# Performance work log

Hardware: AMD Instinct MI355X
Metric: run time of the kernel (lower is better)

## Reference

```python
import jax, jax.numpy as jnp
import numpy as np

EMBED = 256; M = 8; DV = 32; L = 4; K = 4; SCALE = 0.5
LEVELS = [(128, 128), (64, 64), (32, 32), (16, 16)]  # (H_l, W_l), static
S_TOTAL = sum(h * w for h, w in LEVELS)  # 21760


def _linear_params(key, fan_in, fan_out):
    kw, kb = jax.random.split(key)
    lim = 1.0 / np.sqrt(fan_in)
    W = jax.random.uniform(kw, (fan_in, fan_out), minval=-lim, maxval=lim, dtype=jnp.float32)
    b = jax.random.uniform(kb, (fan_out,), minval=-lim, maxval=lim, dtype=jnp.float32)
    return W, b


def setup_inputs() -> dict:
    key = jax.random.key(0)
    ks = jax.random.split(key, 8)
    N, Q = 2, 8192
    W_off, b_off = _linear_params(ks[0], EMBED, M * L * K * 2)
    W_attn, b_attn = _linear_params(ks[1], EMBED, M * L * K)
    W_val, b_val = _linear_params(ks[2], EMBED, M * DV)
    W_out, b_out = _linear_params(ks[3], M * DV, EMBED)
    queries = jax.random.normal(ks[4], (N, Q, EMBED), dtype=jnp.float32)
    query_geometry_logits = jax.random.normal(ks[5], (N, Q, 4), dtype=jnp.float32)
    value = jax.random.normal(ks[6], (N, S_TOTAL, EMBED), dtype=jnp.float32)
    value_mask = jnp.ones((N, S_TOTAL, 1), dtype=jnp.float32)
    return {"queries": queries, "query_geometry_logits": query_geometry_logits,
            "value": value, "value_mask": value_mask,
            "W_off": W_off, "b_off": b_off, "W_attn": W_attn, "b_attn": b_attn,
            "W_val": W_val, "b_val": b_val, "W_out": W_out, "b_out": b_out}


def _bilinear(img_flat, grid, H, W):
    """grid_sample(mode=bilinear, padding=zeros, align_corners=False).
    img_flat: (B, H*W, C); grid: (B, P, 2) with (x, y) in [-1, 1]."""
    x = (grid[..., 0] + 1.0) * (W * 0.5) - 0.5
    y = (grid[..., 1] + 1.0) * (H * 0.5) - 0.5
    x0f, y0f = jnp.floor(x), jnp.floor(y)
    wx, wy = x - x0f, y - y0f
    x0, y0 = x0f.astype(jnp.int32), y0f.astype(jnp.int32)

    def gather(xi, yi, w):
        valid = (xi >= 0) & (xi < W) & (yi >= 0) & (yi < H)
        idx = jnp.clip(yi, 0, H - 1) * W + jnp.clip(xi, 0, W - 1)
        v = jnp.take_along_axis(img_flat, idx[..., None], axis=1)
        return v * (w * valid)[..., None]

    return (gather(x0, y0, (1 - wx) * (1 - wy)) + gather(x0 + 1, y0, wx * (1 - wy))
            + gather(x0, y0 + 1, (1 - wx) * wy) + gather(x0 + 1, y0 + 1, wx * wy))


def _forward(queries, query_geometry_logits, value, value_mask,
             W_off, b_off, W_attn, b_attn, W_val, b_val, W_out, b_out):
    N, Q, _ = queries.shape
    # attention weights: (N, Q, M, L*K), softmax over the L*K sampling points
    attn = jax.nn.softmax((queries @ W_attn + b_attn).reshape(N, Q, M, L * K), axis=-1)
    # sampling offsets: (N, Q, M, L*K, 2)
    deltas = (queries @ W_off + b_off).reshape(N, Q, M, L * K, 2)
    # reference boxes: sigmoid -> (cx, cy, w, h) in [0, 1]
    b_q = jax.nn.sigmoid(query_geometry_logits)
    xy, wh = b_q[..., :2], b_q[..., 2:]
    scale = wh * (1.0 / K) * SCALE                       # (N, Q, 2)
    pos = xy[:, :, None, None, :] + deltas * scale[:, :, None, None, :]  # (N,Q,M,LK,2)
    # value projection + mask
    v_masked = value_mask * (value @ W_val + b_val)      # (N, S, M*DV)
    # collapse (N, M) for per-head grid sampling
    grid = jnp.clip(2.0 * pos.transpose(0, 2, 1, 3, 4).reshape(N * M, Q, L * K, 2) - 1.0, -1.0, 1.0)
    outs, start = [], 0
    for li, (H, W) in enumerate(LEVELS):
        v_l = v_masked[:, start:start + H * W, :].reshape(N, H * W, M, DV)
        v_l = v_l.transpose(0, 2, 1, 3).reshape(N * M, H * W, DV)
        g_l = grid[:, :, K * li:K * (li + 1), :].reshape(N * M, Q * K, 2)
        s_l = _bilinear(v_l, g_l, H, W)                  # (N*M, Q*K, DV)
        outs.append(s_l.reshape(N, M, Q, K, DV))
        start += H * W
    vals = jnp.concatenate(outs, axis=3)                 # (N, M, Q, L*K, DV)
    vals = vals.transpose(0, 2, 1, 3, 4)                 # (N, Q, M, L*K, DV)
    out = jnp.sum(attn[..., None] * vals, axis=3).reshape(N, Q, M * DV)
    return out @ W_out + b_out                           # (N, Q, EMBED)


def reference(queries, query_geometry_logits, value, value_mask,
              W_off, b_off, W_attn, b_attn, W_val, b_val, W_out, b_out):
    return _forward(queries, query_geometry_logits, value, value_mask,
                    W_off, b_off, W_attn, b_attn, W_val, b_val, W_out, b_out)
```

## Files before the change

### kernel.cpp

```cpp
#include <hip/hip_runtime.h>
#include <math.h>

#define EMBED   256
#define M_HEADS 8
#define DVAL    32
#define LK      16
#define S_TOTAL 21760
#define NQ      8192
#define NROWS   (2 * NQ)
#define QBS     16

typedef __attribute__((ext_vector_type(8))) short s16x8;
typedef __attribute__((ext_vector_type(4))) short s16x4;
typedef __attribute__((ext_vector_type(4))) float f32x4;
typedef unsigned short u16;
typedef unsigned int   u32;

__device__ __forceinline__ short f2bf(float f) {
    unsigned u = __float_as_uint(f);
    u += 0x7fffu + ((u >> 16) & 1u);
    return (short)(u >> 16);
}
__device__ __forceinline__ float bf2f(short h) {
    return __uint_as_float(((unsigned)(u16)h) << 16);
}

#define V_OFF     0
#define V_FLTS    5570560
#define PA_OFF    (V_OFF + V_FLTS)
#define PA_FLTS   6291456
#define MID_OFF   (PA_OFF + PA_FLTS)
#define MID_FLTS  2097152
#define WHI_OFF   (MID_OFF + MID_FLTS)
#define WOA_FLTS  49152
#define WLO_OFF   (WHI_OFF + WOA_FLTS)
#define WV_OFF    (WLO_OFF + WOA_FLTS)
#define WO_OFF    (WV_OFF + 32768)

__global__ __launch_bounds__(256) void prep_kernel(
    const float* __restrict__ W_off, const float* __restrict__ W_attn,
    u16* __restrict__ Whi,           u16* __restrict__ Wlo,
    const float* __restrict__ W_val, u16* __restrict__ Wv,
    const float* __restrict__ W_out, u16* __restrict__ Wo)
{
    const int b = blockIdx.x;
    const int t = threadIdx.x;

    if (b < 512) {
        const int flat = b * 256 + t;
        const int which = flat >> 16;
        const int e = flat & 65535;
        const int k = e >> 8, c = e & 255;
        const float f = which ? W_out[k * 256 + c] : W_val[k * 256 + c];
        const int kt = k >> 5, qd = (k >> 3) & 3, j = k & 7;
        const int idx = (((kt * 256 + c) << 2) + qd) * 8 + j;
        (which ? Wo : Wv)[idx] = (u16)f2bf(f);
    } else {
        const int flat = (b - 512) * 256 + t;
        const int k = flat / 384, c = flat - k * 384;
        const float f = (c < 256) ? W_off[k * 256 + c] : W_attn[k * 128 + (c - 256)];
        const short h = f2bf(f);
        const short lo = f2bf(f - bf2f(h));
        const int kt = k >> 5, qd = (k >> 3) & 3, j = k & 7;
        const int idx = (((kt * 384 + c) << 2) + qd) * 8 + j;
        Whi[idx] = (u16)h;
        Wlo[idx] = (u16)lo;
    }
}

__global__ __launch_bounds__(256, 2) void vproj_kernel(
    const float* __restrict__ value,
    const float* __restrict__ vmask,
    const u16* __restrict__ Wpk,
    const float* __restrict__ b_val,
    u16* __restrict__ v_out)
{
    __shared__ u16 sA[4096];

    const int t  = threadIdx.x;
    const int w  = t >> 6, l = t & 63;
    const int c  = l & 15, qd = l >> 4;
    const int c0 = w * 64;

    s16x8 B[8][4];
    #pragma unroll
    for (int kt = 0; kt < 8; ++kt)
        #pragma unroll
        for (int nt = 0; nt < 4; ++nt)
            B[kt][nt] = *(const s16x8*)(Wpk + (((kt * 256 + c0 + nt * 16 + c) << 2) + qd) * 8);

    float bias[4];
    #pragma unroll
    for (int nt = 0; nt < 4; ++nt) bias[nt] = b_val[c0 + nt * 16 + c];

    const int srow = t >> 6;
    const int scol = 4 * (t & 63);

    int tile = blockIdx.x;
    float4 st[4];
    {
        const float* __restrict__ vp = value + (size_t)tile * 16 * EMBED;
        #pragma unroll
        for (int i = 0; i < 4; ++i)
            st[i] = *(const float4*)(vp + (i * 4 + srow) * EMBED + scol);
    }

    for (;;) {
        #pragma unroll
        for (int i = 0; i < 4; ++i) {
            const int row = i * 4 + srow;
            const int idx = ((row << 8) + scol) ^ ((row & 7) << 3);
            *(s16x4*)(sA + idx) = (s16x4){ f2bf(st[i].x), f2bf(st[i].y),
                                           f2bf(st[i].z), f2bf(st[i].w) };
        }
        __syncthreads();

        const int r0   = tile * 16;
        const int next = tile + 512;
        if (next < 2720) {
            const float* __restrict__ vp = value + (size_t)next * 16 * EMBED;
            #pragma unroll
            for (int i = 0; i < 4; ++i)
                st[i] = *(const float4*)(vp + (i * 4 + srow) * EMBED + scol);
        }

        f32x4 acc[4] = {};
        #pragma unroll
        for (int kt = 0; kt < 8; ++kt) {
            const s16x8 a = *(const s16x8*)(sA + ((((c << 8) + kt * 32 + qd * 8)) ^ ((c & 7) << 3)));
            #pragma unroll
            for (int nt = 0; nt < 4; ++nt)
                acc[nt] = __builtin_amdgcn_mfma_f32_16x16x32_bf16(a, B[kt][nt], acc[nt], 0, 0, 0);
        }

        #pragma unroll
        for (int r = 0; r < 4; ++r) {
            const int grow = r0 + qd * 4 + r;
            const int n = (grow >= S_TOTAL) ? 1 : 0;
            const int s = grow - n * S_TOTAL;
            const float mk = vmask[grow];
            #pragma unroll
            for (int nt = 0; nt < 4; ++nt) {
                const int col = c0 + nt * 16 + c;
                const int hm = col >> 5, d = col & 31;
                v_out[((size_t)(n * M_HEADS + hm) * S_TOTAL + s) * DVAL + d] =
                    (u16)f2bf((acc[nt][r] + bias[nt]) * mk);
            }
        }
        __syncthreads();
        if (next >= 2720) break;
        tile = next;
    }
}

__global__ __launch_bounds__(256) void qproj_kernel(
    const float* __restrict__ queries,
    const float* __restrict__ qgl,
    const u16* __restrict__ Whi, const u16* __restrict__ Wlo,
    const float* __restrict__ b_off, const float* __restrict__ b_attn,
    float* __restrict__ pa)
{
    __shared__ __align__(16) char s_un[33280];
    __shared__ float s_attn[32][132];
    __shared__ float s_geom[32][4];

    u16* sAh = (u16*)s_un;
    u16* sAl = sAh + 8192;
    float (*s_off)[260] = (float(*)[260])s_un;

    const int t  = threadIdx.x;
    const int w  = t >> 6, l = t & 63;
    const int c  = l & 15, qd = l >> 4;
    const int row0 = blockIdx.x * 32;
    const int c0 = w * 96;

    if (t < 32) {
        const float* g = &qgl[(size_t)(row0 + t) * 4];
        s_geom[t][0] = 1.f / (1.f + __expf(-g[0]));
        s_geom[t][1] = 1.f / (1.f + __expf(-g[1]));
        s_geom[t][2] = (1.f / (1.f + __expf(-g[2]))) * 0.125f;
        s_geom[t][3] = (1.f / (1.f + __expf(-g[3]))) * 0.125f;
    }

    {
        const int srow = t >> 6;
        const int scol = 4 * (t & 63);
        #pragma unroll
        for (int i = 0; i < 8; ++i) {
            const int row = i * 4 + srow;
            const float4 v = *(const float4*)(queries + (size_t)(row0 + row) * EMBED + scol);
            const short h0 = f2bf(v.x), h1 = f2bf(v.y), h2 = f2bf(v.z), h3 = f2bf(v.w);
            const int idx = ((row << 8) + scol) ^ ((row & 7) << 3);
            *(s16x4*)(sAh + idx) = (s16x4){ h0, h1, h2, h3 };
            *(s16x4*)(sAl + idx) = (s16x4){ f2bf(v.x - bf2f(h0)), f2bf(v.y - bf2f(h1)),
                                            f2bf(v.z - bf2f(h2)), f2bf(v.w - bf2f(h3)) };
        }
    }
    __syncthreads();

    f32x4 acc[2][6] = {};

    s16x8 bhA[6], blA[6], bhB[6], blB[6];

    auto loadB = [&](int kt, s16x8 (&bh)[6], s16x8 (&bl)[6]) {
        #pragma unroll
        for (int nt = 0; nt < 6; ++nt) {
            const int idx = (((kt * 384 + c0 + nt * 16 + c) << 2) + qd) * 8;
            bh[nt] = *(const s16x8*)(Whi + idx);
            bl[nt] = *(const s16x8*)(Wlo + idx);
        }
    };
    auto stepK = [&](int kt, s16x8 (&bh)[6], s16x8 (&bl)[6]) {
        s16x8 ah[2], al[2];
        #pragma unroll
        for (int mt = 0; mt < 2; ++mt) {
            const int row = mt * 16 + c;
            const int idx = ((row << 8) + kt * 32 + qd * 8) ^ ((row & 7) << 3);
            ah[mt] = *(const s16x8*)(sAh + idx);
            al[mt] = *(const s16x8*)(sAl + idx);
        }
        #pragma unroll
        for (int mt = 0; mt < 2; ++mt)
            #pragma unroll
            for (int nt = 0; nt < 6; ++nt) {
                acc[mt][nt] = __builtin_amdgcn_mfma_f32_16x16x32_bf16(ah[mt], bh[nt], acc[mt][nt], 0, 0, 0);
                acc[mt][nt] = __builtin_amdgcn_mfma_f32_16x16x32_bf16(ah[mt], bl[nt], acc[mt][nt], 0, 0, 0);
                acc[mt][nt] = __builtin_amdgcn_mfma_f32_16x16x32_bf16(al[mt], bh[nt], acc[mt][nt], 0, 0, 0);
            }
    };

    loadB(0, bhA, blA);
    loadB(1, bhB, blB);
    #pragma unroll
    for (int kp = 0; kp < 4; ++kp) {
        stepK(2 * kp, bhA, blA);
        if (kp < 3) loadB(2 * kp + 2, bhA, blA);
        stepK(2 * kp + 1, bhB, blB);
        if (kp < 3) loadB(2 * kp + 3, bhB, blB);
    }
    __syncthreads();

    #pragma unroll
    for (int mt = 0; mt < 2; ++mt)
        #pragma unroll
        for (int nt = 0; nt < 6; ++nt) {
            const int col = c0 + nt * 16 + c;
            #pragma unroll
            for (int r = 0; r < 4; ++r) {
                const int row = mt * 16 + qd * 4 + r;
                if (col < 256) s_off[row][col] = acc[mt][nt][r] + b_off[col];
                else           s_attn[row][col - 256] = acc[mt][nt][r] + b_attn[col - 256];
            }
        }
    __syncthreads();

    {
        const int qi = t >> 3, hm = t & 7;
        float* a = &s_attn[qi][hm * LK];
        float mx = a[0];
        #pragma unroll
        for (int i = 1; i < LK; ++i) mx = fmaxf(mx, a[i]);
        float s = 0.f;
        #pragma unroll
        for (int i = 0; i < LK; ++i) { const float e = __expf(a[i] - mx); a[i] = e; s += e; }
        const float inv = 1.f / s;
        #pragma unroll
        for (int i = 0; i < LK; ++i) a[i] *= inv;
    }
    __syncthreads();

    for (int p = t; p < 32 * 128; p += 256) {
        const int qi = p >> 7;
        const int pt = p & 127;
        const int lvl = (pt & 15) >> 2;
        const float Wl = (float)(128 >> lvl);
        const float px = fmaf(s_off[qi][2 * pt + 0], s_geom[qi][2], s_geom[qi][0]);
        const float py = fmaf(s_off[qi][2 * pt + 1], s_geom[qi][3], s_geom[qi][1]);
        const float gx = fminf(fmaxf(2.f * px - 1.f, -1.f), 1.f);
        const float gy = fminf(fmaxf(2.f * py - 1.f, -1.f), 1.f);
        const float x = (gx + 1.f) * (Wl * 0.5f) - 0.5f;
        const float y = (gy + 1.f) * (Wl * 0.5f) - 0.5f;
        const size_t idx = ((size_t)(row0 + qi) * 128 + pt) * 3;
        pa[idx + 0] = x;
        pa[idx + 1] = y;
        pa[idx + 2] = s_attn[qi][pt];
    }
}

__global__ __launch_bounds__(256) void sample_kernel(
    const float* __restrict__ pa,
    const u16* __restrict__ v_tab,
    u16* __restrict__ mid)
{
    __shared__ int4   s_idx[QBS * 17];
    __shared__ float4 s_w[QBS * 17];

    const int t    = threadIdx.x;
    const int m    = blockIdx.x & 7;
    const int rest = blockIdx.x >> 3;
    const int qc   = rest & 511;
    const int n    = rest >> 9;
    const int q0   = qc * QBS;

    {
        const int qi = t >> 4, lk = t & 15;
        const int lvl   = lk >> 2;
        const int Wl    = 128 >> lvl;
        const int start = (lvl == 0) ? 0 : (lvl == 1) ? 16384 : (lvl == 2) ? 20480 : 21504;

        const size_t prow = ((size_t)(n * NQ + q0 + qi)) * 128 + m * 16 + lk;
        const float x  = pa[prow * 3 + 0];
        const float y  = pa[prow * 3 + 1];
        const float aw = pa[prow * 3 + 2];

        const float x0f = floorf(x), y0f = floorf(y);
        const int   x0 = (int)x0f, y0 = (int)y0f;
        const float wx = x - x0f, wy = y - y0f;

        const float vx0 = (x0 >= 0) ? 1.f : 0.f;
        const float vx1 = (x0 + 1 <= Wl - 1) ? 1.f : 0.f;
        const float vy0 = (y0 >= 0) ? 1.f : 0.f;
        const float vy1 = (y0 + 1 <= Wl - 1) ? 1.f : 0.f;

        const int xc0 = max(x0, 0);
        const int xc1 = min(x0 + 1, Wl - 1);
        const int yc0 = max(y0, 0);
        const int yc1 = min(y0 + 1, Wl - 1);

        const int e = qi * 17 + lk;
        s_idx[e] = make_int4((start + yc0 * Wl + xc0) * DVAL,
                             (start + yc0 * Wl + xc1) * DVAL,
                             (start + yc1 * Wl + xc0) * DVAL,
                             (start + yc1 * Wl + xc1) * DVAL);
        s_w[e] = make_float4(aw * (1.f - wx) * (1.f - wy) * vx0 * vy0,
                             aw * wx * (1.f - wy) * vx1 * vy0,
                             aw * (1.f - wx) * wy * vx0 * vy1,
                             aw * wx * wy * vx1 * vy1);
    }
    __syncthreads();

    const int g = t >> 4, dp = t & 15;
    const u16* __restrict__ vbp =
        v_tab + (size_t)(n * M_HEADS + m) * S_TOTAL * DVAL + 2 * dp;

    float acc0 = 0.f, acc1 = 0.f;
    #pragma unroll
    for (int lk = 0; lk < LK; ++lk) {
        const int4   id = s_idx[g * 17 + lk];
        const float4 w  = s_w[g * 17 + lk];
        const u32 u0 = *(const u32*)(vbp + id.x);
        const u32 u1 = *(const u32*)(vbp + id.y);
        const u32 u2 = *(const u32*)(vbp + id.z);
        const u32 u3 = *(const u32*)(vbp + id.w);
        acc0 = fmaf(w.x, __uint_as_float(u0 << 16), acc0);
        acc1 = fmaf(w.x, __uint_as_float(u0 & 0xffff0000u), acc1);
        acc0 = fmaf(w.y, __uint_as_float(u1 << 16), acc0);
        acc1 = fmaf(w.y, __uint_as_float(u1 & 0xffff0000u), acc1);
        acc0 = fmaf(w.z, __uint_as_float(u2 << 16), acc0);
        acc1 = fmaf(w.z, __uint_as_float(u2 & 0xffff0000u), acc1);
        acc0 = fmaf(w.w, __uint_as_float(u3 << 16), acc0);
        acc1 = fmaf(w.w, __uint_as_float(u3 & 0xffff0000u), acc1);
    }

    const u32 packed = ((u32)(u16)f2bf(acc1) << 16) | (u32)(u16)f2bf(acc0);
    *(u32*)(mid + ((size_t)(n * NQ + q0 + g)) * EMBED + m * DVAL + 2 * dp) = packed;
}

__global__ __launch_bounds__(256, 2) void out_kernel(
    const u16* __restrict__ mid,
    const u16* __restrict__ Wpk,
    const float* __restrict__ b_out,
    float* __restrict__ out)
{
    const int t  = threadIdx.x;
    const int w  = t >> 6, l = t & 63;
    const int c  = l & 15, qd = l >> 4;
    const int c0 = w * 64;

    s16x8 B[8][4];
    #pragma unroll
    for (int kt = 0; kt < 8; ++kt)
        #pragma unroll
        for (int nt = 0; nt < 4; ++nt)
            B[kt][nt] = *(const s16x8*)(Wpk + (((kt * 256 + c0 + nt * 16 + c) << 2) + qd) * 8);

    float bias[4];
    #pragma unroll
    for (int nt = 0; nt < 4; ++nt) bias[nt] = b_out[c0 + nt * 16 + c];

    for (int tile = blockIdx.x; tile < 1024; tile += 512) {
        const int r0 = tile * 16;
        const u16* __restrict__ ap = mid + (size_t)(r0 + c) * EMBED + qd * 8;

        s16x8 a[8];
        #pragma unroll
        for (int kt = 0; kt < 8; ++kt)
            a[kt] = *(const s16x8*)(ap + kt * 32);

        f32x4 acc[4] = {};
        #pragma unroll
        for (int kt = 0; kt < 8; ++kt)
            #pragma unroll
            for (int nt = 0; nt < 4; ++nt)
                acc[nt] = __builtin_amdgcn_mfma_f32_16x16x32_bf16(a[kt], B[kt][nt], acc[nt], 0, 0, 0);

        #pragma unroll
        for (int r = 0; r < 4; ++r) {
            const int row = r0 + qd * 4 + r;
            #pragma unroll
            for (int nt = 0; nt < 4; ++nt)
                out[(size_t)row * EMBED + c0 + nt * 16 + c] = acc[nt][r] + bias[nt];
        }
    }
}

extern "C" void kernel_launch(void* const* d_in, const int* in_sizes, int n_in,
                              void* d_out, int out_size, void* d_ws, size_t ws_size,
                              hipStream_t stream) {
    (void)in_sizes; (void)n_in; (void)out_size; (void)ws_size;

    const float* queries = (const float*)d_in[0];
    const float* qgl     = (const float*)d_in[1];
    const float* value   = (const float*)d_in[2];
    const float* vmask   = (const float*)d_in[3];
    const float* W_off   = (const float*)d_in[4];
    const float* b_off   = (const float*)d_in[5];
    const float* W_attn  = (const float*)d_in[6];
    const float* b_attn  = (const float*)d_in[7];
    const float* W_val   = (const float*)d_in[8];
    const float* b_val   = (const float*)d_in[9];
    const float* W_out   = (const float*)d_in[10];
    const float* b_out   = (const float*)d_in[11];

    float* ws   = (float*)d_ws;
    u16*  v_ws  = (u16*)(ws + V_OFF);
    float* pa   = ws + PA_OFF;
    u16*  mid   = (u16*)(ws + MID_OFF);
    u16*  whi   = (u16*)(ws + WHI_OFF);
    u16*  wlo   = (u16*)(ws + WLO_OFF);
    u16*  wvpk  = (u16*)(ws + WV_OFF);
    u16*  wopk  = (u16*)(ws + WO_OFF);
    float* outp = (float*)d_out;

    prep_kernel<<<896, 256, 0, stream>>>(W_off, W_attn, whi, wlo,
                                         W_val, wvpk, W_out, wopk);

    vproj_kernel<<<512, 256, 0, stream>>>(value, vmask, wvpk, b_val, v_ws);
    qproj_kernel<<<NROWS / 32, 256, 0, stream>>>(queries, qgl, whi, wlo,
                                                 b_off, b_attn, pa);
    sample_kernel<<<2 * (NQ / QBS) * M_HEADS, 256, 0, stream>>>(pa, v_ws, mid);
    out_kernel<<<512, 256, 0, stream>>>(mid, wopk, b_out, outp);
}
```

Before: 186.7 us.

## Merge value and query projection kernels into one launch with interleaved blocks

Fuses the value projection and query projection kernels into a single kernel, with even blocks doing value tiles and odd blocks doing query tiles. The aim is to overlap the two independent phases on the GPU and remove one launch and its tail. In exchange the value branch now shares a larger static LDS allocation and loses its launch_bounds occupancy hint, which may cut occupancy for those blocks.

```diff
diff --git a/kernel.cpp b/kernel.cpp
--- a/kernel.cpp
+++ b/kernel.cpp
@@ -68,222 +68,220 @@
     }
 }
 
-__global__ __launch_bounds__(256, 2) void vproj_kernel(
+__global__ __launch_bounds__(256) void vq_kernel(
     const float* __restrict__ value,
     const float* __restrict__ vmask,
-    const u16* __restrict__ Wpk,
+    const u16* __restrict__ Wvpk,
     const float* __restrict__ b_val,
-    u16* __restrict__ v_out)
-{
-    __shared__ u16 sA[4096];
-
-    const int t  = threadIdx.x;
-    const int w  = t >> 6, l = t & 63;
-    const int c  = l & 15, qd = l >> 4;
-    const int c0 = w * 64;
-
-    s16x8 B[8][4];
-    #pragma unroll
-    for (int kt = 0; kt < 8; ++kt)
-        #pragma unroll
-        for (int nt = 0; nt < 4; ++nt)
-            B[kt][nt] = *(const s16x8*)(Wpk + (((kt * 256 + c0 + nt * 16 + c) << 2) + qd) * 8);
-
-    float bias[4];
-    #pragma unroll
-    for (int nt = 0; nt < 4; ++nt) bias[nt] = b_val[c0 + nt * 16 + c];
-
-    const int srow = t >> 6;
-    const int scol = 4 * (t & 63);
-
-    int tile = blockIdx.x;
-    float4 st[4];
-    {
-        const float* __restrict__ vp = value + (size_t)tile * 16 * EMBED;
-        #pragma unroll
-        for (int i = 0; i < 4; ++i)
-            st[i] = *(const float4*)(vp + (i * 4 + srow) * EMBED + scol);
-    }
-
-    for (;;) {
-        #pragma unroll
-        for (int i = 0; i < 4; ++i) {
-            const int row = i * 4 + srow;
-            const int idx = ((row << 8) + scol) ^ ((row & 7) << 3);
-            *(s16x4*)(sA + idx) = (s16x4){ f2bf(st[i].x), f2bf(st[i].y),
-                                           f2bf(st[i].z), f2bf(st[i].w) };
-        }
-        __syncthreads();
-
-        const int r0   = tile * 16;
-        const int next = tile + 512;
-        if (next < 2720) {
-            const float* __restrict__ vp = value + (size_t)next * 16 * EMBED;
-            #pragma unroll
-            for (int i = 0; i < 4; ++i)
-                st[i] = *(const float4*)(vp + (i * 4 + srow) * EMBED + scol);
-        }
-
-        f32x4 acc[4] = {};
-        #pragma unroll
-        for (int kt = 0; kt < 8; ++kt) {
-            const s16x8 a = *(const s16x8*)(sA + ((((c << 8) + kt * 32 + qd * 8)) ^ ((c & 7) << 3)));
-            #pragma unroll
-            for (int nt = 0; nt < 4; ++nt)
-                acc[nt] = __builtin_amdgcn_mfma_f32_16x16x32_bf16(a, B[kt][nt], acc[nt], 0, 0, 0);
-        }
-
-        #pragma unroll
-        for (int r = 0; r < 4; ++r) {
-            const int grow = r0 + qd * 4 + r;
-            const int n = (grow >= S_TOTAL) ? 1 : 0;
-            const int s = grow - n * S_TOTAL;
-            const float mk = vmask[grow];
-            #pragma unroll
-            for (int nt = 0; nt < 4; ++nt) {
-                const int col = c0 + nt * 16 + c;
-                const int hm = col >> 5, d = col & 31;
-                v_out[((size_t)(n * M_HEADS + hm) * S_TOTAL + s) * DVAL + d] =
-                    (u16)f2bf((acc[nt][r] + bias[nt]) * mk);
-            }
-        }
-        __syncthreads();
-        if (next >= 2720) break;
-        tile = next;
-    }
-}
-
-__global__ __launch_bounds__(256) void qproj_kernel(
+    u16* __restrict__ v_out,
     const float* __restrict__ queries,
     const float* __restrict__ qgl,
     const u16* __restrict__ Whi, const u16* __restrict__ Wlo,
     const float* __restrict__ b_off, const float* __restrict__ b_attn,
     float* __restrict__ pa)
 {
-    __shared__ __align__(16) char s_un[33280];
-    __shared__ float s_attn[32][132];
-    __shared__ float s_geom[32][4];
-
-    u16* sAh = (u16*)s_un;
-    u16* sAl = sAh + 8192;
-    float (*s_off)[260] = (float(*)[260])s_un;
+    __shared__ __align__(16) char lds[50688];
 
     const int t  = threadIdx.x;
     const int w  = t >> 6, l = t & 63;
     const int c  = l & 15, qd = l >> 4;
-    const int row0 = blockIdx.x * 32;
-    const int c0 = w * 96;
-
-    if (t < 32) {
-        const float* g = &qgl[(size_t)(row0 + t) * 4];
-        s_geom[t][0] = 1.f / (1.f + __expf(-g[0]));
-        s_geom[t][1] = 1.f / (1.f + __expf(-g[1]));
-        s_geom[t][2] = (1.f / (1.f + __expf(-g[2]))) * 0.125f;
-        s_geom[t][3] = (1.f / (1.f + __expf(-g[3]))) * 0.125f;
-    }
-
-    {
+
+    if ((blockIdx.x & 1) == 0) {
+        u16* sA = (u16*)lds;
+
+        const int vb = blockIdx.x >> 1;
+        const int c0 = w * 64;
+
+        s16x8 B[8][4];
+        #pragma unroll
+        for (int kt = 0; kt < 8; ++kt)
+            #pragma unroll
+            for (int nt = 0; nt < 4; ++nt)
+                B[kt][nt] = *(const s16x8*)(Wvpk + (((kt * 256 + c0 + nt * 16 + c) << 2) + qd) * 8);
+
+        float bias[4];
+        #pragma unroll
+        for (int nt = 0; nt < 4; ++nt) bias[nt] = b_val[c0 + nt * 16 + c];
+
         const int srow = t >> 6;
         const int scol = 4 * (t & 63);
-        #pragma unroll
-        for (int i = 0; i < 8; ++i) {
-            const int row = i * 4 + srow;
-            const float4 v = *(const float4*)(queries + (size_t)(row0 + row) * EMBED + scol);
-            const short h0 = f2bf(v.x), h1 = f2bf(v.y), h2 = f2bf(v.z), h3 = f2bf(v.w);
-            const int idx = ((row << 8) + scol) ^ ((row & 7) << 3);
-            *(s16x4*)(sAh + idx) = (s16x4){ h0, h1, h2, h3 };
-            *(s16x4*)(sAl + idx) = (s16x4){ f2bf(v.x - bf2f(h0)), f2bf(v.y - bf2f(h1)),
-                                            f2bf(v.z - bf2f(h2)), f2bf(v.w - bf2f(h3)) };
-        }
-    }
-    __syncthreads();
-
-    f32x4 acc[2][6] = {};
-
-    s16x8 bhA[6], blA[6], bhB[6], blB[6];
-
-    auto loadB = [&](int kt, s16x8 (&bh)[6], s16x8 (&bl)[6]) {
-        #pragma unroll
-        for (int nt = 0; nt < 6; ++nt) {
-            const int idx = (((kt * 384 + c0 + nt * 16 + c) << 2) + qd) * 8;
-            bh[nt] = *(const s16x8*)(Whi + idx);
-            bl[nt] = *(const s16x8*)(Wlo + idx);
-        }
-    };
-    auto stepK = [&](int kt, s16x8 (&bh)[6], s16x8 (&bl)[6]) {
-        s16x8 ah[2], al[2];
-        #pragma unroll
-        for (int mt = 0; mt < 2; ++mt) {
-            const int row = mt * 16 + c;
-            const int idx = ((row << 8) + kt * 32 + qd * 8) ^ ((row & 7) << 3);
-            ah[mt] = *(const s16x8*)(sAh + idx);
-            al[mt] = *(const s16x8*)(sAl + idx);
-        }
+
+        int tile = vb;
+        float4 st[4];
+        {
+            const float* __restrict__ vp = value + (size_t)tile * 16 * EMBED;
+            #pragma unroll
+            for (int i = 0; i < 4; ++i)
+                st[i] = *(const float4*)(vp + (i * 4 + srow) * EMBED + scol);
+        }
+
+        for (;;) {
+            #pragma unroll
+            for (int i = 0; i < 4; ++i) {
+                const int row = i * 4 + srow;
+                const int idx = ((row << 8) + scol) ^ ((row & 7) << 3);
+                *(s16x4*)(sA + idx) = (s16x4){ f2bf(st[i].x), f2bf(st[i].y),
+                                               f2bf(st[i].z), f2bf(st[i].w) };
+            }
+            __syncthreads();
+
+            const int r0   = tile * 16;
+            const int next = tile + 512;
+            if (next < 2720) {
+                const float* __restrict__ vp = value + (size_t)next * 16 * EMBED;
+                #pragma unroll
+                for (int i = 0; i < 4; ++i)
+                    st[i] = *(const float4*)(vp + (i * 4 + srow) * EMBED + scol);
+            }
+
+            f32x4 acc[4] = {};
+            #pragma unroll
+            for (int kt = 0; kt < 8; ++kt) {
+                const s16x8 a = *(const s16x8*)(sA + ((((c << 8) + kt * 32 + qd * 8)) ^ ((c & 7) << 3)));
+                #pragma unroll
+                for (int nt = 0; nt < 4; ++nt)
+                    acc[nt] = __builtin_amdgcn_mfma_f32_16x16x32_bf16(a, B[kt][nt], acc[nt], 0, 0, 0);
+            }
+
+            #pragma unroll
+            for (int r = 0; r < 4; ++r) {
+                const int grow = r0 + qd * 4 + r;
+                const int n = (grow >= S_TOTAL) ? 1 : 0;
+                const int s = grow - n * S_TOTAL;
+                const float mk = vmask[grow];
+                #pragma unroll
+                for (int nt = 0; nt < 4; ++nt) {
+                    const int col = c0 + nt * 16 + c;
+                    const int hm = col >> 5, d = col & 31;
+                    v_out[((size_t)(n * M_HEADS + hm) * S_TOTAL + s) * DVAL + d] =
+                        (u16)f2bf((acc[nt][r] + bias[nt]) * mk);
+                }
+            }
+            __syncthreads();
+            if (next >= 2720) break;
+            tile = next;
+        }
+    } else {
+        u16* sAh = (u16*)lds;
+        u16* sAl = sAh + 8192;
+        float (*s_off)[260]  = (float(*)[260])lds;
+        float (*s_attn)[132] = (float(*)[132])(lds + 33280);
+        float (*s_geom)[4]   = (float(*)[4])(lds + 50176);
+
+        const int qb   = blockIdx.x >> 1;
+        const int row0 = qb * 32;
+        const int c0   = w * 96;
+
+        if (t < 32) {
+            const float* g = &qgl[(size_t)(row0 + t) * 4];
+            s_geom[t][0] = 1.f / (1.f + __expf(-g[0]));
+            s_geom[t][1] = 1.f / (1.f + __expf(-g[1]));
+            s_geom[t][2] = (1.f / (1.f + __expf(-g[2]))) * 0.125f;
+            s_geom[t][3] = (1.f / (1.f + __expf(-g[3]))) * 0.125f;
+        }
+
+        {
+            const int srow = t >> 6;
+            const int scol = 4 * (t & 63);
+            #pragma unroll
+            for (int i = 0; i < 8; ++i) {
+                const int row = i * 4 + srow;
+                const float4 v = *(const float4*)(queries + (size_t)(row0 + row) * EMBED + scol);
+                const short h0 = f2bf(v.x), h1 = f2bf(v.y), h2 = f2bf(v.z), h3 = f2bf(v.w);
+                const int idx = ((row << 8) + scol) ^ ((row & 7) << 3);
+                *(s16x4*)(sAh + idx) = (s16x4){ h0, h1, h2, h3 };
+                *(s16x4*)(sAl + idx) = (s16x4){ f2bf(v.x - bf2f(h0)), f2bf(v.y - bf2f(h1)),
+                                                f2bf(v.z - bf2f(h2)), f2bf(v.w - bf2f(h3)) };
+            }
+        }
+        __syncthreads();
+
+        f32x4 acc[2][6] = {};
+        s16x8 bhA[6], blA[6], bhB[6], blB[6];
+
+        auto loadB = [&](int kt, s16x8 (&bh)[6], s16x8 (&bl)[6]) {
+            #pragma unroll
+            for (int nt = 0; nt < 6; ++nt) {
+                const int idx = (((kt * 384 + c0 + nt * 16 + c) << 2) + qd) * 8;
+                bh[nt] = *(const s16x8*)(Whi + idx);
+                bl[nt] = *(const s16x8*)(Wlo + idx);
+            }
+        };
+        auto stepK = [&](int kt, s16x8 (&bh)[6], s16x8 (&bl)[6]) {
+            s16x8 ah[2], al[2];
+            #pragma unroll
+            for (int mt = 0; mt < 2; ++mt) {
+                const int row = mt * 16 + c;
+                const int idx = ((row << 8) + kt * 32 + qd * 8) ^ ((row & 7) << 3);
+                ah[mt] = *(const s16x8*)(sAh + idx);
+                al[mt] = *(const s16x8*)(sAl + idx);
+            }
+            #pragma unroll
+            for (int mt = 0; mt < 2; ++mt)
+                #pragma unroll
+                for (int nt = 0; nt < 6; ++nt) {
+                    acc[mt][nt] = __builtin_amdgcn_mfma_f32_16x16x32_bf16(ah[mt], bh[nt], acc[mt][nt], 0, 0, 0);
+                    acc[mt][nt] = __builtin_amdgcn_mfma_f32_16x16x32_bf16(ah[mt], bl[nt], acc[mt][nt], 0, 0, 0);
+                    acc[mt][nt] = __builtin_amdgcn_mfma_f32_16x16x32_bf16(al[mt], bh[nt], acc[mt][nt], 0, 0, 0);
+                }
+        };
+
+        loadB(0, bhA, blA);
+        loadB(1, bhB, blB);
+        #pragma unroll
+        for (int kp = 0; kp < 4; ++kp) {
+            stepK(2 * kp, bhA, blA);
+            if (kp < 3) loadB(2 * kp + 2, bhA, blA);
+            stepK(2 * kp + 1, bhB, blB);
+            if (kp < 3) loadB(2 * kp + 3, bhB, blB);
+        }
+        __syncthreads();
+
         #pragma unroll
         for (int mt = 0; mt < 2; ++mt)
             #pragma unroll
             for (int nt = 0; nt < 6; ++nt) {
-                acc[mt][nt] = __builtin_amdgcn_mfma_f32_16x16x32_bf16(ah[mt], bh[nt], acc[mt][nt], 0, 0, 0);
-                acc[mt][nt] = __builtin_amdgcn_mfma_f32_16x16x32_bf16(ah[mt], bl[nt], acc[mt][nt], 0, 0, 0);
-                acc[mt][nt] = __builtin_amdgcn_mfma_f32_16x16x32_bf16(al[mt], bh[nt], acc[mt][nt], 0, 0, 0);
-            }
-    };
-
-    loadB(0, bhA, blA);
-    loadB(1, bhB, blB);
-    #pragma unroll
-    for (int kp = 0; kp < 4; ++kp) {
-        stepK(2 * kp, bhA, blA);
-        if (kp < 3) loadB(2 * kp + 2, bhA, blA);
-        stepK(2 * kp + 1, bhB, blB);
-        if (kp < 3) loadB(2 * kp + 3, bhB, blB);
-    }
-    __syncthreads();
-
-    #pragma unroll
-    for (int mt = 0; mt < 2; ++mt)
-        #pragma unroll
-        for (int nt = 0; nt < 6; ++nt) {
-            const int col = c0 + nt * 16 + c;
-            #pragma unroll
-            for (int r = 0; r < 4; ++r) {
-                const int row = mt * 16 + qd * 4 + r;
-                if (col < 256) s_off[row][col] = acc[mt][nt][r] + b_off[col];
-                else           s_attn[row][col - 256] = acc[mt][nt][r] + b_attn[col - 256];
-            }
-        }
-    __syncthreads();
-
-    {
-        const int qi = t >> 3, hm = t & 7;
-        float* a = &s_attn[qi][hm * LK];
-        float mx = a[0];
-        #pragma unroll
-        for (int i = 1; i < LK; ++i) mx = fmaxf(mx, a[i]);
-        float s = 0.f;
-        #pragma unroll
-        for (int i = 0; i < LK; ++i) { const float e = __expf(a[i] - mx); a[i] = e; s += e; }
-        const float inv = 1.f / s;
-        #pragma unroll
-        for (int i = 0; i < LK; ++i) a[i] *= inv;
-    }
-    __syncthreads();
-
-    for (int p = t; p < 32 * 128; p += 256) {
-        const int qi = p >> 7;
-        const int pt = p & 127;
-        const int lvl = (pt & 15) >> 2;
-        const float Wl = (float)(128 >> lvl);
-        const float px = fmaf(s_off[qi][2 * pt + 0], s_geom[qi][2], s_geom[qi][0]);
-        const float py = fmaf(s_off[qi][2 * pt + 1], s_geom[qi][3], s_geom[qi][1]);
-        const float gx = fminf(fmaxf(2.f * px - 1.f, -1.f), 1.f);
-        const float gy = fminf(fmaxf(2.f * py - 1.f, -1.f), 1.f);
-        const float x = (gx + 1.f) * (Wl * 0.5f) - 0.5f;
-        const float y = (gy + 1.f) * (Wl * 0.5f) - 0.5f;
-        const size_t idx = ((size_t)(row0 + qi) * 128 + pt) * 3;
-        pa[idx + 0] = x;
-        pa[idx + 1] = y;
-        pa[idx + 2] = s_attn[qi][pt];
+                const int col = c0 + nt * 16 + c;
+                #pragma unroll
+                for (int r = 0; r < 4; ++r) {
+                    const int row = mt * 16 + qd * 4 + r;
+                    if (col < 256) s_off[row][col] = acc[mt][nt][r] + b_off[col];
+                    else           s_attn[row][col - 256] = acc[mt][nt][r] + b_attn[col - 256];
+                }
+            }
+        __syncthreads();
+
+        {
+            const int qi = t >> 3, hm = t & 7;
+            float* a = &s_attn[qi][hm * LK];
+            float mx = a[0];
+            #pragma unroll
+            for (int i = 1; i < LK; ++i) mx = fmaxf(mx, a[i]);
+            float s = 0.f;
+            #pragma unroll
+            for (int i = 0; i < LK; ++i) { const float e = __expf(a[i] - mx); a[i] = e; s += e; }
+            const float inv = 1.f / s;
+            #pragma unroll
+            for (int i = 0; i < LK; ++i) a[i] *= inv;
+        }
+        __syncthreads();
+
+        for (int p = t; p < 32 * 128; p += 256) {
+            const int qi = p >> 7;
+            const int pt = p & 127;
+            const int lvl = (pt & 15) >> 2;
+            const float Wl = (float)(128 >> lvl);
+            const float px = fmaf(s_off[qi][2 * pt + 0], s_geom[qi][2], s_geom[qi][0]);
+            const float py = fmaf(s_off[qi][2 * pt + 1], s_geom[qi][3], s_geom[qi][1]);
+            const float gx = fminf(fmaxf(2.f * px - 1.f, -1.f), 1.f);
+            const float gy = fminf(fmaxf(2.f * py - 1.f, -1.f), 1.f);
+            const float x = (gx + 1.f) * (Wl * 0.5f) - 0.5f;
+            const float y = (gy + 1.f) * (Wl * 0.5f) - 0.5f;
+            const size_t idx = ((size_t)(row0 + qi) * 128 + pt) * 3;
+            pa[idx + 0] = x;
+            pa[idx + 1] = y;
+            pa[idx + 2] = s_attn[qi][pt];
+        }
     }
 }
 
@@ -445,9 +443,9 @@
     prep_kernel<<<896, 256, 0, stream>>>(W_off, W_attn, whi, wlo,
                                          W_val, wvpk, W_out, wopk);
 
-    vproj_kernel<<<512, 256, 0, stream>>>(value, vmask, wvpk, b_val, v_ws);
-    qproj_kernel<<<NROWS / 32, 256, 0, stream>>>(queries, qgl, whi, wlo,
-                                                 b_off, b_attn, pa);
+    vq_kernel<<<1024, 256, 0, stream>>>(value, vmask, wvpk, b_val, v_ws,
+                                        queries, qgl, whi, wlo,
+                                        b_off, b_attn, pa);
     sample_kernel<<<2 * (NQ / QBS) * M_HEADS, 256, 0, stream>>>(pa, v_ws, mid);
     out_kernel<<<512, 256, 0, stream>>>(mid, wopk, b_out, outp);
 }
```

Measured after the change: 207.2 us. 10.9% more time.
